# Kernel optimization log

Measured on AMD Instinct MI355X. Metric: run time of the kernel, lower is better.

The kernel has to match this reference:

```python
import jax, jax.numpy as jnp
import numpy as np

B, N_IN, D_IN, N_OUT, D_OUT = 16, 256, 128, 128, 64
W_INIT_CONST = float(np.sqrt(N_OUT / (D_IN * N_IN)))


def setup_inputs() -> dict:
    key = jax.random.key(0)
    k1, k2, k3 = jax.random.split(key, 3)
    x = jax.random.normal(k1, (B, N_IN, D_IN), dtype=jnp.float32)
    current_act = jax.random.uniform(k2, (B, N_IN), dtype=jnp.float32)
    W = W_INIT_CONST * jax.random.normal(k3, (N_IN, D_IN, N_OUT, D_OUT), dtype=jnp.float32)
    return {"input": x, "current_act": current_act, "W": W, "num_iter": 1}


def reference(input, current_act, W, num_iter):
    scale = 1.0 / np.sqrt(D_OUT)
    # votes[b,n,m,d] = sum_a input[b,n,a] * W[n,a,m,d]  -- the big bilinear product,
    # computed once and reused for score computation and the final weighted reduce.
    votes = jnp.einsum('bna,namd->bnmd', input, W)  # [B, N_IN, N_OUT, D_OUT]

    # next_capsule_value is None -> uniform query_key = softmax(zeros) = 1/N_OUT
    ncv = votes.sum(axis=1) / N_OUT  # [B, N_OUT, D_OUT]

    # next_act is None -> mean activation broadcast to all output capsules
    next_act = jnp.broadcast_to(current_act.mean(axis=1, keepdims=True), (B, N_OUT))

    # attention-like routing coefficients
    scores = jnp.einsum('bnmd,bmd->bnm', votes, ncv) * scale  # [B, N_IN, N_OUT]
    qk = jax.nn.softmax(scores, axis=2) * next_act[:, None, :]
    qk = qk / (qk.sum(axis=2, keepdims=True) + 1e-10)

    # weighted reduce of votes, gated by input activations
    next_capsule_value = jnp.einsum('bnm,bn,bnmd->bmd', qk, current_act, votes)
    return (next_capsule_value, next_act, qk)
```

## Files before the change

kernel.cpp:

```cpp
#include <hip/hip_runtime.h>
#include <hip/hip_bf16.h>
#include <cstdint>


#define BB 16
#define N_IN 256
#define D_IN 128
#define N_OUT 128
#define D_OUT 64
#define MD (N_OUT * D_OUT)
#define NPB 2
#define NCH 32

__global__ __launch_bounds__(256) void pass0_xT(
    const float* __restrict__ x, float* __restrict__ xT)
{
    const int idx = blockIdx.x * 256 + threadIdx.x;
    const int b = idx & 15;
    const int a = (idx >> 4) & 127;
    const int n = idx >> 11;
    xT[idx] = x[((size_t)b * N_IN + n) * D_IN + a];
}

__global__ __launch_bounds__(256, 2) void pass1_votes(
    const float* __restrict__ xT, const float* __restrict__ W,
    uint2* __restrict__ votes4)
{
    __shared__ float xs[NPB * D_IN * BB];
    const int t = threadIdx.x;
    const int chunk = blockIdx.x;
    const int ng = blockIdx.y;
    const int j = chunk * 1024 + t * 4;

    {
        const float4* src = reinterpret_cast<const float4*>(xT + ((size_t)ng * NPB << 11));
        float4* dst = reinterpret_cast<float4*>(xs);
#pragma unroll
        for (int r = 0; r < 4; ++r) dst[r * 256 + t] = src[r * 256 + t];
    }
    __syncthreads();

    for (int ni = 0; ni < NPB; ++ni) {
        const int n = ng * NPB + ni;
        const float4* __restrict__ Wp =
            reinterpret_cast<const float4*>(W + (size_t)n * D_IN * MD + j);

        float acc[BB][4];
#pragma unroll
        for (int b = 0; b < BB; ++b) {
            acc[b][0] = 0.f; acc[b][1] = 0.f; acc[b][2] = 0.f; acc[b][3] = 0.f;
        }

#pragma unroll 4
        for (int a = 0; a < D_IN; ++a) {
            const float4 w = Wp[(size_t)a * (MD / 4)];
            const float4* xa = reinterpret_cast<const float4*>(xs + (ni * D_IN + a) * BB);
            const float4 x0 = xa[0], x1 = xa[1], x2 = xa[2], x3 = xa[3];
            const float xv[BB] = {x0.x, x0.y, x0.z, x0.w, x1.x, x1.y, x1.z, x1.w,
                                  x2.x, x2.y, x2.z, x2.w, x3.x, x3.y, x3.z, x3.w};
#pragma unroll
            for (int b = 0; b < BB; ++b) {
                acc[b][0] = fmaf(xv[b], w.x, acc[b][0]);
                acc[b][1] = fmaf(xv[b], w.y, acc[b][1]);
                acc[b][2] = fmaf(xv[b], w.z, acc[b][2]);
                acc[b][3] = fmaf(xv[b], w.w, acc[b][3]);
            }
        }

#pragma unroll
        for (int b = 0; b < BB; ++b) {
            union { __hip_bfloat16 h[4]; uint2 u; } pk;
            pk.h[0] = __float2bfloat16(acc[b][0]);
            pk.h[1] = __float2bfloat16(acc[b][1]);
            pk.h[2] = __float2bfloat16(acc[b][2]);
            pk.h[3] = __float2bfloat16(acc[b][3]);
            votes4[(((size_t)b * N_IN + n) * MD + j) >> 2] = pk.u;
        }
    }
}

__global__ __launch_bounds__(256) void pass_ncv_part(
    const uint32_t* __restrict__ votes2, float* __restrict__ ncv_part)
{
    const int t = threadIdx.x;
    const int jc = blockIdx.x;
    const int nh = blockIdx.y;
    const int b  = blockIdx.z;
    const int j = jc * 1024 + t * 4;

    const uint2* vp = reinterpret_cast<const uint2*>(votes2) +
                      ((((size_t)b * N_IN + (size_t)nh * 64) * MD + j) >> 2);
    float s0 = 0.f, s1 = 0.f, s2 = 0.f, s3 = 0.f;
#pragma unroll 8
    for (int n = 0; n < 64; ++n) {
        const uint2 u = vp[(size_t)n * (MD / 4)];
        s0 += __uint_as_float(u.x << 16);
        s1 += __uint_as_float(u.x & 0xffff0000u);
        s2 += __uint_as_float(u.y << 16);
        s3 += __uint_as_float(u.y & 0xffff0000u);
    }
    float4 o; o.x = s0; o.y = s1; o.z = s2; o.w = s3;
    *reinterpret_cast<float4*>(ncv_part + ((size_t)nh * BB + b) * MD + j) = o;
}

__global__ __launch_bounds__(256) void pass3_route(
    const __hip_bfloat16* __restrict__ votes, const float* __restrict__ ncv_part,
    const float* __restrict__ act, float* __restrict__ out_part,
    float* __restrict__ next_act_out, float* __restrict__ qk_out)
{
    __shared__ float red[4];
    __shared__ float aw[4];
    const int t = threadIdx.x;
    const int b = blockIdx.x;
    const int nc = blockIdx.y;
    const int m = t >> 1;
    const int half = t & 1;

    float av = act[b * N_IN + t];
#pragma unroll
    for (int off = 32; off; off >>= 1) av += __shfl_xor(av, off);
    if ((t & 63) == 0) aw[t >> 6] = av;
    __syncthreads();
    const float amean = (aw[0] + aw[1] + aw[2] + aw[3]) * (1.f / 256.f);
    const float qs = amean / (amean + 1e-10f);
    if (nc == 0 && half == 0) next_act_out[b * N_OUT + m] = amean;

    float nv[32], oacc[32];
    {
        const float4* p0 = reinterpret_cast<const float4*>(ncv_part + ((size_t)0 * BB + b) * MD + t * 32);
        const float4* p1 = reinterpret_cast<const float4*>(ncv_part + ((size_t)1 * BB + b) * MD + t * 32);
        const float4* p2 = reinterpret_cast<const float4*>(ncv_part + ((size_t)2 * BB + b) * MD + t * 32);
        const float4* p3 = reinterpret_cast<const float4*>(ncv_part + ((size_t)3 * BB + b) * MD + t * 32);
#pragma unroll
        for (int q = 0; q < 8; ++q) {
            const float4 a0 = p0[q], a1 = p1[q], a2 = p2[q], a3 = p3[q];
            nv[4 * q + 0] = (a0.x + a1.x) + (a2.x + a3.x);
            nv[4 * q + 1] = (a0.y + a1.y) + (a2.y + a3.y);
            nv[4 * q + 2] = (a0.z + a1.z) + (a2.z + a3.z);
            nv[4 * q + 3] = (a0.w + a1.w) + (a2.w + a3.w);
        }
#pragma unroll
        for (int i = 0; i < 32; ++i) { nv[i] *= (1.f / (float)N_OUT); oacc[i] = 0.f; }
    }

    const uint4* vbase = reinterpret_cast<const uint4*>(
        votes + (size_t)b * ((size_t)N_IN * MD) + (size_t)(nc * 8) * MD + t * 32);
    const size_t nstride = MD / 8;

    uint4 buf[4];
#pragma unroll
    for (int q = 0; q < 4; ++q) buf[q] = vbase[q];

    for (int ni = 0; ni < 8; ++ni) {
        const int n = nc * 8 + ni;
        float vv[32];
#pragma unroll
        for (int q = 0; q < 4; ++q) {
            const uint32_t ww[4] = {buf[q].x, buf[q].y, buf[q].z, buf[q].w};
#pragma unroll
            for (int k = 0; k < 4; ++k) {
                vv[8 * q + 2 * k]     = __uint_as_float(ww[k] << 16);
                vv[8 * q + 2 * k + 1] = __uint_as_float(ww[k] & 0xffff0000u);
            }
        }
        if (ni < 7) {
            const uint4* vn = vbase + (size_t)(ni + 1) * nstride;
#pragma unroll
            for (int q = 0; q < 4; ++q) buf[q] = vn[q];
        }

        float p0 = 0.f, p1 = 0.f, p2 = 0.f, p3 = 0.f;
#pragma unroll
        for (int i = 0; i < 8; ++i) {
            p0 = fmaf(vv[4 * i + 0], nv[4 * i + 0], p0);
            p1 = fmaf(vv[4 * i + 1], nv[4 * i + 1], p1);
            p2 = fmaf(vv[4 * i + 2], nv[4 * i + 2], p2);
            p3 = fmaf(vv[4 * i + 3], nv[4 * i + 3], p3);
        }
        float sp = (p0 + p1) + (p2 + p3);
        sp += __shfl_xor(sp, 1);
        sp *= 0.125f;

        const float p = __expf(sp);
        float s = p;
#pragma unroll
        for (int off = 32; off; off >>= 1) s += __shfl_xor(s, off);
        if ((t & 63) == 0) red[t >> 6] = s;
        __syncthreads();
        const float ssum = (red[0] + red[1] + red[2] + red[3]) * 0.5f;
        __syncthreads();

        const float qk = (p / ssum) * qs;
        if (half == 0) qk_out[((size_t)(b * N_IN + n) << 7) + m] = qk;

        const float c = qk * act[b * N_IN + n];
#pragma unroll
        for (int i = 0; i < 32; ++i) oacc[i] = fmaf(c, vv[i], oacc[i]);
    }

    float4* op = reinterpret_cast<float4*>(out_part + ((size_t)nc * BB + b) * MD + t * 32);
#pragma unroll
    for (int q = 0; q < 8; ++q) {
        float4 o; o.x = oacc[4 * q]; o.y = oacc[4 * q + 1];
        o.z = oacc[4 * q + 2]; o.w = oacc[4 * q + 3];
        op[q] = o;
    }
}

__global__ __launch_bounds__(256) void combine_out0(
    const float* __restrict__ out_part, float* __restrict__ out0)
{
    const int idx = blockIdx.x * 256 + threadIdx.x;
    const int b = idx >> 11;
    const int v4 = idx & 2047;
    const float4* p = reinterpret_cast<const float4*>(out_part);
    float4 s = {0.f, 0.f, 0.f, 0.f};
#pragma unroll 8
    for (int nc = 0; nc < NCH; ++nc) {
        const float4 f = p[((size_t)nc * BB + b) * (MD / 4) + v4];
        s.x += f.x; s.y += f.y; s.z += f.z; s.w += f.w;
    }
    reinterpret_cast<float4*>(out0)[idx] = s;
}

extern "C" void kernel_launch(void* const* d_in, const int* in_sizes, int n_in,
                              void* d_out, int out_size, void* d_ws, size_t ws_size,
                              hipStream_t stream)
{
    const float* x   = (const float*)d_in[0];
    const float* act = (const float*)d_in[1];
    const float* W   = (const float*)d_in[2];

    float* out      = (float*)d_out;
    float* out0     = out;
    float* next_act = out + 131072;
    float* qk_out   = out + 131072 + 2048;

    __hip_bfloat16* votes = (__hip_bfloat16*)d_ws;
    float* ncv_part = (float*)((char*)d_ws + (size_t)67108864);
    float* out_part = (float*)((char*)d_ws + (size_t)67108864 + 2097152);
    float* xT       = (float*)((char*)d_ws + (size_t)67108864 + 2097152 + 16777216);

    pass0_xT<<<2048, 256, 0, stream>>>(x, xT);
    pass1_votes<<<dim3(8, 128), 256, 0, stream>>>(xT, W, (uint2*)votes);
    pass_ncv_part<<<dim3(8, 4, 16), 256, 0, stream>>>((const uint32_t*)votes, ncv_part);
    pass3_route<<<dim3(16, NCH), 256, 0, stream>>>(votes, ncv_part, act, out_part,
                                                   next_act, qk_out);
    combine_out0<<<128, 256, 0, stream>>>(out_part, out0);
}
```

Baseline: 272.0 us.

## Widen votes GEMM per-thread tile to 8 columns and double routing chunks

The votes kernel now has each thread compute 8 output columns instead of 4, loading two float4 W values per step and writing 16-byte bf16 stores. Its grid is halved in x and the two-blocks-per-SM launch bound is dropped. Separately, the routing pass splits N_IN into 64 chunks of 4 instead of 32 chunks of 8, which gives more blocks for parallelism but doubles the partial outputs, so the workspace offset grows. The wider tile reuses each LDS x load across more FMAs but uses more registers and gives fewer blocks in the votes GEMM, which may reduce occupancy.

```diff
diff --git a/kernel.cpp b/kernel.cpp
--- a/kernel.cpp
+++ b/kernel.cpp
@@ -10,7 +10,8 @@
 #define D_OUT 64
 #define MD (N_OUT * D_OUT)
 #define NPB 2
-#define NCH 32
+#define JW 8
+#define NCH 64
 
 __global__ __launch_bounds__(256) void pass0_xT(
     const float* __restrict__ x, float* __restrict__ xT)
@@ -22,15 +23,15 @@
     xT[idx] = x[((size_t)b * N_IN + n) * D_IN + a];
 }
 
-__global__ __launch_bounds__(256, 2) void pass1_votes(
+__global__ __launch_bounds__(256) void pass1_votes(
     const float* __restrict__ xT, const float* __restrict__ W,
-    uint2* __restrict__ votes4)
+    uint4* __restrict__ votes8)
 {
     __shared__ float xs[NPB * D_IN * BB];
     const int t = threadIdx.x;
     const int chunk = blockIdx.x;
     const int ng = blockIdx.y;
-    const int j = chunk * 1024 + t * 4;
+    const int j = chunk * 2048 + t * 8;
 
     {
         const float4* src = reinterpret_cast<const float4*>(xT + ((size_t)ng * NPB << 11));
@@ -45,36 +46,39 @@
         const float4* __restrict__ Wp =
             reinterpret_cast<const float4*>(W + (size_t)n * D_IN * MD + j);
 
-        float acc[BB][4];
-#pragma unroll
-        for (int b = 0; b < BB; ++b) {
-            acc[b][0] = 0.f; acc[b][1] = 0.f; acc[b][2] = 0.f; acc[b][3] = 0.f;
-        }
-
-#pragma unroll 4
+        float acc[BB][JW];
+#pragma unroll
+        for (int b = 0; b < BB; ++b)
+#pragma unroll
+            for (int k = 0; k < JW; ++k) acc[b][k] = 0.f;
+
+#pragma unroll 2
         for (int a = 0; a < D_IN; ++a) {
-            const float4 w = Wp[(size_t)a * (MD / 4)];
+            const float4 w0 = Wp[(size_t)a * (MD / 4)];
+            const float4 w1 = Wp[(size_t)a * (MD / 4) + 1];
             const float4* xa = reinterpret_cast<const float4*>(xs + (ni * D_IN + a) * BB);
             const float4 x0 = xa[0], x1 = xa[1], x2 = xa[2], x3 = xa[3];
             const float xv[BB] = {x0.x, x0.y, x0.z, x0.w, x1.x, x1.y, x1.z, x1.w,
                                   x2.x, x2.y, x2.z, x2.w, x3.x, x3.y, x3.z, x3.w};
 #pragma unroll
             for (int b = 0; b < BB; ++b) {
-                acc[b][0] = fmaf(xv[b], w.x, acc[b][0]);
-                acc[b][1] = fmaf(xv[b], w.y, acc[b][1]);
-                acc[b][2] = fmaf(xv[b], w.z, acc[b][2]);
-                acc[b][3] = fmaf(xv[b], w.w, acc[b][3]);
+                acc[b][0] = fmaf(xv[b], w0.x, acc[b][0]);
+                acc[b][1] = fmaf(xv[b], w0.y, acc[b][1]);
+                acc[b][2] = fmaf(xv[b], w0.z, acc[b][2]);
+                acc[b][3] = fmaf(xv[b], w0.w, acc[b][3]);
+                acc[b][4] = fmaf(xv[b], w1.x, acc[b][4]);
+                acc[b][5] = fmaf(xv[b], w1.y, acc[b][5]);
+                acc[b][6] = fmaf(xv[b], w1.z, acc[b][6]);
+                acc[b][7] = fmaf(xv[b], w1.w, acc[b][7]);
             }
         }
 
 #pragma unroll
         for (int b = 0; b < BB; ++b) {
-            union { __hip_bfloat16 h[4]; uint2 u; } pk;
-            pk.h[0] = __float2bfloat16(acc[b][0]);
-            pk.h[1] = __float2bfloat16(acc[b][1]);
-            pk.h[2] = __float2bfloat16(acc[b][2]);
-            pk.h[3] = __float2bfloat16(acc[b][3]);
-            votes4[(((size_t)b * N_IN + n) * MD + j) >> 2] = pk.u;
+            union { __hip_bfloat16 h[8]; uint4 u; } pk;
+#pragma unroll
+            for (int k = 0; k < JW; ++k) pk.h[k] = __float2bfloat16(acc[b][k]);
+            votes8[(((size_t)b * N_IN + n) * MD + j) >> 3] = pk.u;
         }
     }
 }
@@ -144,15 +148,15 @@
     }
 
     const uint4* vbase = reinterpret_cast<const uint4*>(
-        votes + (size_t)b * ((size_t)N_IN * MD) + (size_t)(nc * 8) * MD + t * 32);
+        votes + (size_t)b * ((size_t)N_IN * MD) + (size_t)(nc * 4) * MD + t * 32);
     const size_t nstride = MD / 8;
 
     uint4 buf[4];
 #pragma unroll
     for (int q = 0; q < 4; ++q) buf[q] = vbase[q];
 
-    for (int ni = 0; ni < 8; ++ni) {
-        const int n = nc * 8 + ni;
+    for (int ni = 0; ni < 4; ++ni) {
+        const int n = nc * 4 + ni;
         float vv[32];
 #pragma unroll
         for (int q = 0; q < 4; ++q) {
@@ -163,7 +167,7 @@
                 vv[8 * q + 2 * k + 1] = __uint_as_float(ww[k] & 0xffff0000u);
             }
         }
-        if (ni < 7) {
+        if (ni < 3) {
             const uint4* vn = vbase + (size_t)(ni + 1) * nstride;
 #pragma unroll
             for (int q = 0; q < 4; ++q) buf[q] = vn[q];
@@ -239,10 +243,10 @@
     __hip_bfloat16* votes = (__hip_bfloat16*)d_ws;
     float* ncv_part = (float*)((char*)d_ws + (size_t)67108864);
     float* out_part = (float*)((char*)d_ws + (size_t)67108864 + 2097152);
-    float* xT       = (float*)((char*)d_ws + (size_t)67108864 + 2097152 + 16777216);
+    float* xT       = (float*)((char*)d_ws + (size_t)67108864 + 2097152 + 33554432);
 
     pass0_xT<<<2048, 256, 0, stream>>>(x, xT);
-    pass1_votes<<<dim3(8, 128), 256, 0, stream>>>(xT, W, (uint2*)votes);
+    pass1_votes<<<dim3(4, 128), 256, 0, stream>>>(xT, W, (uint4*)votes);
     pass_ncv_part<<<dim3(8, 4, 16), 256, 0, stream>>>((const uint32_t*)votes, ncv_part);
     pass3_route<<<dim3(16, NCH), 256, 0, stream>>>(votes, ncv_part, act, out_part,
                                                    next_act, qk_out);
```

Result: slower. 284.2 us (+4.5%).
